# Kernel optimization log

Measured on AMD Instinct MI355X. Metric: run time of the kernel, lower is better.

Reference implementation:

```python
import jax, jax.numpy as jnp
import numpy as np
import math

B = 1024      # graphs
N = 64        # nodes per graph (padded, masked by node_mask)
BN = B * N    # total nodes
EPG = 192     # directed edges per graph
E = B * EPG


def setup_inputs() -> dict:
    key = jax.random.key(0)
    ks = jax.random.split(key, 40)

    def nrm(k, shp, s=0.02):
        return (jax.random.normal(k, shp) * s).astype(jnp.float32)

    mol_batch_x = jax.random.normal(ks[0], (BN, 19), dtype=jnp.float32)
    offs = jnp.arange(B, dtype=jnp.int32) * N
    src = jax.random.randint(ks[1], (B, EPG), 0, N, dtype=jnp.int32) + offs[:, None]
    dst = jax.random.randint(ks[2], (B, EPG), 0, N, dtype=jnp.int32) + offs[:, None]
    mol_batch_edge_index = jnp.stack([src.reshape(-1), dst.reshape(-1)], axis=0)
    mol_batch_batch = jnp.repeat(jnp.arange(B, dtype=jnp.int32), N)
    text_features = jax.random.normal(ks[3], (B, 300), dtype=jnp.float32)
    timesteps = jax.random.uniform(ks[4], (B,), minval=0.0, maxval=1000.0, dtype=jnp.float32)
    node_mask = (jax.random.uniform(ks[5], (B, N)) > 0.1).astype(jnp.float32)

    p = {
        'W_tr': nrm(ks[6], (19, 300)),   'b_tr': jnp.zeros((300,), jnp.float32),
        'W_c1': nrm(ks[7], (300, 600)),  'b_c1': jnp.zeros((600,), jnp.float32),
        'W_c2': nrm(ks[8], (600, 600)),  'b_c2': jnp.zeros((600,), jnp.float32),
        'W_c3': nrm(ks[9], (600, 600)),  'b_c3': jnp.zeros((600,), jnp.float32),
        'W_h1': nrm(ks[10], (600, 600)), 'b_h1': jnp.zeros((600,), jnp.float32),
        'W_h2': nrm(ks[11], (600, 600)), 'b_h2': jnp.zeros((600,), jnp.float32),
        'W_h3': nrm(ks[12], (600, 300)), 'b_h3': jnp.zeros((300,), jnp.float32),
        'ln_g': jnp.ones((300,), jnp.float32), 'ln_b': jnp.zeros((300,), jnp.float32),
        'W_t1': nrm(ks[13], (128, 512)), 'b_t1': jnp.zeros((512,), jnp.float32),
        'W_t2': nrm(ks[14], (512, 512)), 'b_t2': jnp.zeros((512,), jnp.float32),
        'W_e':  nrm(ks[15], (512, 3000)), 'b_e': jnp.zeros((3000,), jnp.float32),
    }
    return dict(mol_batch_x=mol_batch_x, mol_batch_edge_index=mol_batch_edge_index,
                mol_batch_batch=mol_batch_batch, text_features=text_features,
                timesteps=timesteps, node_mask=node_mask, **p)


def timestep_embedding(t, dim=128, max_period=10000.0):
    half = dim // 2
    freqs = jnp.exp(-math.log(max_period) * jnp.arange(half, dtype=jnp.float32) / half)
    args = t[:, None] * freqs[None]                 # [B, half]
    return jnp.concatenate([jnp.cos(args), jnp.sin(args)], axis=-1)  # [B, dim]


def gcn_conv(x, W, b, src, dst, num_nodes):
    # PyG GCNConv: D^{-1/2} (A + I) D^{-1/2} X W + b, edge weights 1
    h = x @ W                                             # [BN, F]
    deg = jnp.zeros((num_nodes,), h.dtype).at[dst].add(1.0) + 1.0  # in-degree + self-loop
    inv_sqrt = jax.lax.rsqrt(deg)
    coef = inv_sqrt[src] * inv_sqrt[dst]                  # [E]
    agg = jax.ops.segment_sum(h[src] * coef[:, None], dst, num_segments=num_nodes)
    return agg + h * (1.0 / deg)[:, None] + b             # self-loop norm = 1/deg


def global_mean_pool(x, batch, num_graphs):
    sums = jax.ops.segment_sum(x, batch, num_segments=num_graphs)
    cnts = jax.ops.segment_sum(jnp.ones((x.shape[0],), x.dtype), batch, num_segments=num_graphs)
    return sums / jnp.maximum(cnts, 1.0)[:, None]


def layer_norm(x, g, b, eps=1e-5):
    mu = jnp.mean(x, axis=-1, keepdims=True)
    var = jnp.mean(jnp.square(x - mu), axis=-1, keepdims=True)
    return (x - mu) * jax.lax.rsqrt(var + eps) * g + b


def reference(mol_batch_x, mol_batch_edge_index, mol_batch_batch, text_features,
              timesteps, node_mask, W_tr, b_tr, W_c1, b_c1, W_c2, b_c2, W_c3, b_c3,
              W_h1, b_h1, W_h2, b_h2, W_h3, b_h3, ln_g, ln_b,
              W_t1, b_t1, W_t2, b_t2, W_e, b_e):
    num_nodes = mol_batch_x.shape[0]
    num_graphs = node_mask.shape[0]
    src, dst = mol_batch_edge_index[0], mol_batch_edge_index[1]

    # FiLM conditioning from timestep embedding
    emb = jax.nn.relu(timestep_embedding(timesteps, 128) @ W_t1 + b_t1) @ W_t2 + b_t2  # [B,512]
    emb_out = jax.nn.relu(emb) @ W_e + b_e                                             # [B,3000]
    s1, t1 = emb_out[:, 0:600], emb_out[:, 600:1200]
    s2, t2 = emb_out[:, 1200:1800], emb_out[:, 1800:2400]
    s3, t3 = emb_out[:, 2400:2700], emb_out[:, 2700:3000]

    # node transform + mask
    x = mol_batch_x @ W_tr + b_tr                     # [BN, 300]
    x = x * node_mask.reshape(-1, 1)

    # GCN stack
    x = jax.nn.relu(gcn_conv(x, W_c1, b_c1, src, dst, num_nodes))
    x = jax.nn.relu(gcn_conv(x, W_c2, b_c2, src, dst, num_nodes))
    x = gcn_conv(x, W_c3, b_c3, src, dst, num_nodes)  # [BN, 600]

    g = global_mean_pool(x, mol_batch_batch, num_graphs)  # [B, 600]
    g = jax.nn.relu(g @ W_h1 + b_h1)
    g = g * (1.0 + s1) + t1
    g = jax.nn.relu(g @ W_h2 + b_h2)
    g = g * (1.0 + s2) + t2
    g = g @ W_h3 + b_h3                                # [B, 300]
    g = g * (1.0 + s3) + t3
    g = layer_norm(g, ln_g, ln_b)
    return (g, text_features)
```

## Files before the change

### kernel.cpp

```cpp
#include <hip/hip_runtime.h>
#include <hip/hip_bf16.h>
#include <cstdint>
#include <cstddef>

static constexpr int B   = 1024;
static constexpr int N   = 64;
static constexpr int BN  = B * N;
static constexpr int EPG = 192;
static constexpr int E   = B * EPG;
static constexpr int FP  = 608;
static constexpr int KP1 = 320;
static constexpr int PMS = 80;
static constexpr int NCONV = 2560;

typedef __hip_bfloat16 bf16;
typedef __bf16 bf16x8 __attribute__((ext_vector_type(8)));
typedef __bf16 bf16x4 __attribute__((ext_vector_type(4)));
typedef float  f32x4  __attribute__((ext_vector_type(4)));

__device__ __forceinline__ void storeC(float* p, float v) { *p = v; }
__device__ __forceinline__ void storeC(bf16* p, float v) { *p = __float2bfloat16(v); }

__device__ __forceinline__ void llds16(const void* g, void* l) {
    __builtin_amdgcn_global_load_lds(
        (const __attribute__((address_space(1))) unsigned int*)g,
        (__attribute__((address_space(3))) unsigned int*)l,
        16, 0, 0);
}

template<bool RELU, bool FILM, typename CT>
__device__ __forceinline__ void g64_tile(
    const bf16* __restrict__ A, int lda,
    const bf16* __restrict__ Bt, int ldb,
    const float* __restrict__ bias,
    CT* __restrict__ C, int ldc, int Ncap,
    const bf16* __restrict__ fS, const bf16* __restrict__ fT, int fstride,
    int K, int m0, int n0, __bf16* As, __bf16* Bs, int tid)
{
    const int lane = tid & 63;
    const int w    = tid >> 6;
    const int wn   = w * 32;
    const int l15  = lane & 15;
    const int lhi  = lane >> 4;

    f32x4 acc[4][2] = {};

    for (int k0 = 0; k0 < K; k0 += 32) {
        {
            int row = tid >> 2, kc = tid & 3;
            char* la = (char*)As + (size_t)(w * 64) * 16;
            llds16(A + (size_t)(m0 + row) * lda + k0 + kc * 8, la);
        }
        #pragma unroll
        for (int t = 0; t < 2; ++t) {
            int ci  = t * 256 + tid;
            int row = ci >> 2, kc = ci & 3;
// ... 2 lines not shown
        }
        asm volatile("s_waitcnt vmcnt(0)" ::: "memory");
        __syncthreads();

        bf16x8 af[4], bg[2];
        #pragma unroll
        for (int i = 0; i < 4; ++i)
            af[i] = *(bf16x8*)(As + (i * 16 + l15) * 32 + lhi * 8);
        #pragma unroll
        for (int j = 0; j < 2; ++j)
            bg[j] = *(bf16x8*)(Bs + (wn + j * 16 + l15) * 32 + lhi * 8);
        #pragma unroll
        for (int i = 0; i < 4; ++i)
            #pragma unroll
            for (int j = 0; j < 2; ++j)
                acc[i][j] = __builtin_amdgcn_mfma_f32_16x16x32_bf16(
                    af[i], bg[j], acc[i][j], 0, 0, 0);
        __syncthreads();
    }

    #pragma unroll
    for (int i = 0; i < 4; ++i) {
        #pragma unroll
        for (int j = 0; j < 2; ++j) {
            int col = n0 + wn + j * 16 + l15;
            if (col < Ncap) {
                float bv = bias ? bias[col] : 0.f;
                #pragma unroll
                for (int e = 0; e < 4; ++e) {
                    int row = m0 + i * 16 + lhi * 4 + e;
                    float v = acc[i][j][e] + bv;
                    if (RELU) v = fmaxf(v, 0.f);
                    if (FILM) {
                        float sv = __bfloat162float(fS[(size_t)row * fstride + col]);
                        float tv = __bfloat162float(fT[(size_t)row * fstride + col]);
                        v = v * (1.f + sv) + tv;
                    }
                    storeC(&C[(size_t)row * ldc + col], v);
                }
            }
        }
    }
}

__device__ __attribute__((noinline)) void guest_g64(
    const bf16* gA, int glda, const bf16* gBt, int gldb,
    const float* gbias, bf16* gC, int gldc, int gNcap, int gK, int gnt,
    int t, char* lds, int tid)
{
    int mt2 = t / gnt, nt2 = t % gnt;
    g64_tile<true, false, bf16>(gA, glda, gBt, gldb, gbias, gC, gldc, gNcap,
                                nullptr, nullptr, 0, gK, mt2 * 64, nt2 * 128,
                                (__bf16*)lds, (__bf16*)(lds + 4096), tid);
}

template<bool RELU, bool FILM, typename CT>
__global__ __launch_bounds__(256) void gemm64(
    const bf16* __restrict__ A, int lda,
    const bf16* __restrict__ Bt, int ldb,
    const float* __restrict__ bias,
    CT* __restrict__ C, int ldc, int Ncap,
    const bf16* __restrict__ fS, const bf16* __restrict__ fT, int fstride,
    int K)
{
    __shared__ __align__(16) __bf16 As[64 * 32];
    __shared__ __align__(16) __bf16 Bs[128 * 32];
    g64_tile<RELU, FILM, CT>(A, lda, Bt, ldb, bias, C, ldc, Ncap,
                             fS, fT, fstride, K,
                             blockIdx.x * 64, blockIdx.y * 128, As, Bs,
                             threadIdx.x);
}

__global__ __launch_bounds__(256) void k_two_gemms(
    const bf16* __restrict__ A2b, const bf16* __restrict__ Wet,
    const float* __restrict__ b_e, bf16* __restrict__ EO,
    const bf16* __restrict__ Yv, const bf16* __restrict__ Wb3,
    const float* __restrict__ b_c3, bf16* __restrict__ G0)
{
    __shared__ __align__(16) __bf16 As[64 * 32];
    __shared__ __align__(16) __bf16 Bs[128 * 32];
    int bid = blockIdx.x;
    if (bid < 384) {
        int mt = bid / 24, nt = bid % 24;
        g64_tile<false, false, bf16>(A2b, 512, Wet, 512, b_e, EO, 3000, 3000,
                                     nullptr, nullptr, 0, 512,
                                     mt * 64, nt * 128, As, Bs, threadIdx.x);
    } else {
        int t = bid - 384;
        int mt = t / 5, nt = t % 5;
        g64_tile<false, false, bf16>(Yv, FP, Wb3, FP, b_c3, G0, FP, 600,
                                     nullptr, nullptr, 0, FP,
                                     mt * 64, nt * 128, As, Bs, threadIdx.x);
    }
}

__global__ __launch_bounds__(256) void conv1_gemm(
    const bf16* __restrict__ A,
    const bf16* __restrict__ Bt,
    const float* __restrict__ bias,
    bf16* __restrict__ X1,
    const bf16* __restrict__ gA, int glda,
    const bf16* __restrict__ gBt, int gldb,
    const float* __restrict__ gbias,
    bf16* __restrict__ gC, int gldc, int gNcap, int gK, int gnt)
{
    __shared__ __align__(16) char regA[17408];
    const int tid = threadIdx.x;
    const int bid = blockIdx.x;

    if (bid >= NCONV) {
        guest_g64(gA, glda, gBt, gldb, gbias, gC, gldc, gNcap, gK, gnt,
                  bid - NCONV, regA, tid);
        return;
    }

    __bf16* As = (__bf16*)regA;
    __bf16* Bs = (__bf16*)(regA + 8192);

    const int lane = tid & 63;
    const int w    = tid >> 6;
    const int wm   = (w & 1) * 64;
    const int wn   = (w >> 1) * 64;
    const int l15  = lane & 15;
    const int lhi  = lane >> 4;

    const int lid = bid >> 3;
    const int mt  = (bid & 7) * 64 + lid / 5;
    const int nt  = lid % 5;
    const int m0  = mt * 128;
    const int n0  = nt * 128;

    f32x4 acc[4][4] = {};
    for (int k0 = 0; k0 < KP1; k0 += 32) {
        #pragma unroll
        for (int t = 0; t < 2; ++t) {
            int ci  = t * 256 + w * 64 + lane;
            int row = ci >> 2, kc = ci & 3;
            char* la = (char*)As + (size_t)(t * 256 + w * 64) * 16;
            char* lb = (char*)Bs + (size_t)(t * 256 + w * 64) * 16;
            llds16(A  + (size_t)(m0 + row) * KP1 + k0 + kc * 8, la);
            llds16(Bt + (size_t)(n0 + row) * KP1 + k0 + kc * 8, lb);
        }
        asm volatile("s_waitcnt vmcnt(0)" ::: "memory");
        __syncthreads();

        bf16x8 af[4], bg[4];
        #pragma unroll
        for (int i = 0; i < 4; ++i)
            af[i] = *(bf16x8*)(As + (wm + i * 16 + l15) * 32 + lhi * 8);
        #pragma unroll
        for (int j = 0; j < 4; ++j)
            bg[j] = *(bf16x8*)(Bs + (wn + j * 16 + l15) * 32 + lhi * 8);
        #pragma unroll
        for (int i = 0; i < 4; ++i)
            #pragma unroll
            for (int j = 0; j < 4; ++j)
                acc[i][j] = __builtin_amdgcn_mfma_f32_16x16x32_bf16(
                    af[i], bg[j], acc[i][j], 0, 0, 0);
        __syncthreads();
    }

    #pragma unroll
    for (int i = 0; i < 4; ++i)
        #pragma unroll
        for (int j = 0; j < 4; ++j) {
            int col = n0 + wn + j * 16 + l15;
            if (col < FP) {
                float bv = (col < 600) ? bias[col] : 0.f;
                #pragma unroll
                for (int e = 0; e < 4; ++e) {
                    int row = m0 + wm + i * 16 + lhi * 4 + e;
                    float v = fmaxf(acc[i][j][e] + bv, 0.f);
                    X1[(size_t)row * FP + col] = __float2bfloat16(v);
                }
            }
        }
}

__global__ __launch_bounds__(256) void conv_fused_q(
    const bf16* __restrict__ A, int lda, int K,
    const bf16* __restrict__ Bt, int ldb,
    const bf16* __restrict__ Pmg,
    const float* __restrict__ bias,
    const float* __restrict__ qv,
    bf16* __restrict__ Y,
    const bf16* __restrict__ gA, int glda,
    const bf16* __restrict__ gBt, int gldb,
    const float* __restrict__ gbias,
    bf16* __restrict__ gC, int gldc, int gNcap, int gK, int gnt)
{
    __shared__ __align__(16) char regA[17408];
    __shared__ __align__(16) __bf16 Pm[128 * PMS];
    __shared__ float s_q[128];

    const int tid = threadIdx.x;
    const int bid = blockIdx.x;

    if (bid >= NCONV) {
        guest_g64(gA, glda, gBt, gldb, gbias, gC, gldc, gNcap, gK, gnt,
                  bid - NCONV, regA, tid);
        return;
    }

    __bf16* As = (__bf16*)regA;
    __bf16* Bs = (__bf16*)(regA + 8192);
    __bf16* Ts = (__bf16*)regA;

    const int lane = tid & 63;
    const int w    = tid >> 6;
    const int wm   = (w & 1) * 64;
    const int wn   = (w >> 1) * 64;
    const int l15  = lane & 15;
    const int lhi  = lane >> 4;

    const int lid = bid >> 3;
    const int mt  = (bid & 7) * 64 + lid / 5;
    const int nt  = lid % 5;
    const int m0  = mt * 128;
    const int n0  = nt * 128;

    #pragma unroll
    for (int i = 0; i < 5; ++i) {
        int cbase = w * 320 + i * 64;
        llds16(Pmg + (size_t)mt * (128 * PMS) + (size_t)(cbase + lane) * 8,
               (char*)Pm + (size_t)cbase * 16);
    }
// ... 37 lines not shown
            #pragma unroll
            for (int i = 0; i < 4; ++i)
                #pragma unroll
                for (int j = 0; j < 4; ++j) {
                    int c_local = j * 16 + l15;
                    int rbase   = wm + i * 16 + lhi * 4;
                    bf16x4 pk;
                    #pragma unroll
                    for (int e = 0; e < 4; ++e) pk[e] = (__bf16)acc[i][j][e];
                    *(bf16x4*)(Ts + c_local * 136 + rbase) = pk;
                }
        }
        __syncthreads();

        f32x4 acc2[4][2] = {};
        #pragma unroll
        for (int k0 = 0; k0 < 64; k0 += 32) {
            bf16x8 pa[4], hb[2];
            #pragma unroll
            for (int i = 0; i < 4; ++i)
                pa[i] = *(bf16x8*)(Pm + (g * 64 + i * 16 + l15) * PMS + k0 + lhi * 8);
            #pragma unroll
            for (int j = 0; j < 2; ++j)
                hb[j] = *(bf16x8*)(Ts + (nb * 32 + j * 16 + l15) * 136
                                      + g * 64 + k0 + lhi * 8);
            #pragma unroll
            for (int i = 0; i < 4; ++i)
                #pragma unroll
                for (int j = 0; j < 2; ++j)
                    acc2[i][j] = __builtin_amdgcn_mfma_f32_16x16x32_bf16(
                        pa[i], hb[j], acc2[i][j], 0, 0, 0);
        }
        #pragma unroll
        for (int j = 0; j < 2; ++j) {
            int col = n0 + h * 64 + nb * 32 + j * 16 + l15;
            float bv = (col < 600) ? bias[col] : 0.f;
            float yp = 0.f;
            #pragma unroll
            for (int i = 0; i < 4; ++i)
                #pragma unroll
                for (int e = 0; e < 4; ++e) {
                    float v = fmaxf(acc2[i][j][e] + bv, 0.f);
                    yp += s_q[g * 64 + i * 16 + lhi * 4 + e] * v;
                }
            yp += __shfl_xor(yp, 16, 64);
            yp += __shfl_xor(yp, 32, 64);
            if (lhi == 0 && col < FP)
                Y[(size_t)(mt * 2 + g) * FP + col] = __float2bfloat16(yp);
        }
        __syncthreads();
    }
}

struct WtJob  { const float* src; bf16* dst; int Ksrc, Nsrc, Kp, Np, blk0; };
struct PrepArgs {
    WtJob j[9];
    int nwt, te0, pp0, xtr0;
    const int*   ei;
    const float* ts;
    const float* xin; const float* Wtr; const float* btr; const float* mask;
    bf16* TE; bf16* Pmg; float* qv; bf16* PX0;
};

__global__ __launch_bounds__(256) void k_prep(PrepArgs a)
{
    __shared__ __align__(16) char sm[35840];
    const int bx  = blockIdx.x;
    const int tid = threadIdx.x;

    if (bx < a.nwt) {
        int ji = 0;
        while (ji < 8 && bx >= a.j[ji + 1].blk0) ++ji;
        WtJob jb = a.j[ji];
        int t  = bx - jb.blk0;
        int kt = (jb.Kp + 63) >> 6;
        int ti = t % kt, tj = t / kt;
        int kg0 = ti * 64, ng0 = tj * 64;
        float (*T)[65] = (float(*)[65])sm;
        #pragma unroll 4
        for (int r = 0; r < 16; ++r) {
            int kl = (tid >> 6) + r * 4, nl = tid & 63;
            int kg = kg0 + kl, ng = ng0 + nl;
            T[kl][nl] = (kg < jb.Ksrc && ng < jb.Nsrc)
                        ? jb.src[(size_t)kg * jb.Nsrc + ng] : 0.f;
        }
        __syncthreads();
        #pragma unroll 4
        for (int r = 0; r < 16; ++r) {
            int nl = (tid >> 6) + r * 4, kl = tid & 63;
            int ng = ng0 + nl, kg = kg0 + kl;
            if (ng < jb.Np && kg < jb.Kp)
                jb.dst[(size_t)ng * jb.Kp + kg] = __float2bfloat16(T[kl][nl]);
        }
    } else if (bx < a.pp0) {
        int idx = (bx - a.te0) * 256 + tid;
        int b = idx >> 7, jj = idx & 127;
        float tt = a.ts[b];
        int h = jj & 63;
        float freq = expf(-9.210340371976184f * (float)h / 64.f);
        float ang = tt * freq;
        a.TE[idx] = __float2bfloat16((jj < 64) ? cosf(ang) : sinf(ang));
    } else if (bx < a.xtr0) {
        int pr = bx - a.pp0;
        float* Pf   = (float*)sm;
        int*   cnt  = (int*)(sm + 32768);
        float* sQ   = (float*)(sm + 33280);
        float* sI   = (float*)(sm + 33792);
        float* sIvd = (float*)(sm + 34304);

        for (int idx = tid; idx < 8192; idx += 256) Pf[idx] = 0.f;
        if (tid < 128) cnt[tid] = 0;
        __syncthreads();
        for (int e = tid; e < 2 * EPG; e += 256) {
            int g  = (e >= EPG);
            int eg = (2 * pr + g) * EPG + (e - g * EPG);
            int ld = (a.ei[E + eg] & 63) + g * 64;
            atomicAdd(&cnt[ld], 1);
        }
        __syncthreads();
        if (tid < 128) {
            float d = (float)cnt[tid] + 1.0f;
            float iv = 1.f / d;
            sIvd[tid] = iv;
            sI[tid]   = rsqrtf(d);
            sQ[tid]   = iv;
        }
        __syncthreads();
        for (int e = tid; e < 2 * EPG; e += 256) {
            int g   = (e >= EPG);
            int eg  = (2 * pr + g) * EPG + (e - g * EPG);
            int lsl = a.ei[eg] & 63;
            int ldl = a.ei[E + eg] & 63;
            float cf = sI[g * 64 + lsl] * sI[g * 64 + ldl];
            atomicAdd(&Pf[(g * 64 + ldl) * 64 + lsl], cf);
            atomicAdd(&sQ[g * 64 + lsl], cf);
        }
        __syncthreads();
        if (tid < 128) {
            Pf[tid * 64 + (tid & 63)] += sIvd[tid];
            a.qv[pr * 128 + tid] = sQ[tid] * (1.f / 64.f);
        }
        __syncthreads();
        for (int idx = tid; idx < 128 * PMS; idx += 256) {
            int r = idx / PMS, k = idx - r * PMS;
            float v = (k < 64) ? Pf[r * 64 + k] : 0.f;
            a.Pmg[(size_t)pr * (128 * PMS) + idx] = __float2bfloat16(v);
        }
    } else {
        int g = bx - a.xtr0;
        float* Pf  = (float*)sm;
        float* Ws  = (float*)sm;
        float* xm  = (float*)(sm + 23104);
        float* xa  = (float*)(sm + 28224);
        float* isqv= (float*)(sm + 33344);
        float* ivdv= (float*)(sm + 33600);
        int*   cnt = (int*)  (sm + 33856);
        float* sb  = (float*)(sm + 34112);

        for (int idx = tid; idx < 4096; idx += 256) Pf[idx] = 0.f;
        if (tid < 64) cnt[tid] = 0;
        __syncthreads();
        for (int e = tid; e < EPG; e += 256)
            atomicAdd(&cnt[a.ei[E + g * EPG + e] & 63], 1);
        __syncthreads();
        if (tid < 64) {
            float d = (float)cnt[tid] + 1.0f;
            ivdv[tid] = 1.f / d;
            isqv[tid] = rsqrtf(d);
        }
        __syncthreads();
        for (int e = tid; e < EPG; e += 256) {
            int ls = a.ei[g * EPG + e] & 63;
            int ld = a.ei[E + g * EPG + e] & 63;
            atomicAdd(&Pf[ld * 64 + ls], isqv[ls] * isqv[ld]);
        }
        for (int idx = tid; idx < 64 * 20; idx += 256) {
            int n = idx / 20, j = idx - n * 20;
            float mv = a.mask[g * 64 + n];
            xm[idx] = (j < 19) ? mv * a.xin[(size_t)(g * 64 + n) * 19 + j] : mv;
        }
        __syncthreads();
        if (tid < 64) Pf[tid * 64 + tid] += ivdv[tid];
        __syncthreads();
        for (int idx = tid; idx < 64 * 20; idx += 256) {
            int r = idx / 20, j = idx - r * 20;
            float s = 0.f;
            #pragma unroll 8
            for (int s2 = 0; s2 < 64; ++s2)
                s += Pf[r * 64 + s2] * xm[s2 * 20 + j];
            xa[idx] = s;
        }
        __syncthreads();
        for (int idx = tid; idx < 19 * 304; idx += 256) {
            int k = idx / 304, c = idx - k * 304;
            Ws[idx] = (c < 300) ? a.Wtr[k * 300 + c] : 0.f;
        }
        for (int c = tid; c < 304; c += 256)
            sb[c] = (c < 300) ? a.btr[c] : 0.f;
        __syncthreads();
        int n  = tid >> 2;
        int c0 = tid & 3;
        float ba = xa[n * 20 + 19];
        for (int c = c0; c < 304; c += 4) {
            float acc = ba * sb[c];
            #pragma unroll
            for (int k = 0; k < 19; ++k)
                acc += xa[n * 20 + k] * Ws[k * 304 + c];
            a.PX0[(size_t)(g * 64 + n) * KP1 + c] = __float2bfloat16(acc);
        }
        bf16x8 z = {};
        for (int idx = tid; idx < 64 * 2; idx += 256) {
            int nn = idx >> 1, jv = idx & 1;
            *(bf16x8*)((__bf16*)a.PX0 + (size_t)(g * 64 + nn) * KP1 + 304 + jv * 8) = z;
        }
    }
}

__global__ __launch_bounds__(256) void k_ln_copy(const float* __restrict__ G,
                                                 const float* __restrict__ lg,
                                                 const float* __restrict__ lb,
                                                 const float* __restrict__ text,
                                                 float* __restrict__ out)
{
    int r = blockIdx.x;
    int tid = threadIdx.x;
    __shared__ float red[4];
    __shared__ float smu, svar;

    float v0 = (tid < 300) ? G[r * 300 + tid] : 0.f;
    float v1 = (tid + 256 < 300) ? G[r * 300 + tid + 256] : 0.f;
    float s = v0 + v1;
    #pragma unroll
    for (int o = 32; o > 0; o >>= 1) s += __shfl_down(s, o, 64);
    if ((tid & 63) == 0) red[tid >> 6] = s;
    __syncthreads();
    if (tid == 0) smu = (red[0] + red[1] + red[2] + red[3]) * (1.f / 300.f);
    __syncthreads();
    float mu = smu;
    float d0 = (tid < 300) ? v0 - mu : 0.f;
    float d1 = (tid + 256 < 300) ? v1 - mu : 0.f;
    s = d0 * d0 + d1 * d1;
    #pragma unroll
    for (int o = 32; o > 0; o >>= 1) s += __shfl_down(s, o, 64);
    if ((tid & 63) == 0) red[tid >> 6] = s;
    __syncthreads();
    if (tid == 0) svar = (red[0] + red[1] + red[2] + red[3]) * (1.f / 300.f);
    __syncthreads();
    float rstd = rsqrtf(svar + 1e-5f);
    if (tid < 300)
        out[r * 300 + tid] = d0 * rstd * lg[tid] + lb[tid];
    if (tid + 256 < 300)
        out[r * 300 + tid + 256] = d1 * rstd * lg[tid + 256] + lb[tid + 256];
    float* o2 = out + (size_t)B * 300;
    for (int c = tid; c < 300; c += 256)
        o2[(size_t)r * 300 + c] = text[(size_t)r * 300 + c];
}

extern "C" void kernel_launch(void* const* d_in, const int* in_sizes, int n_in,
                              void* d_out, int out_size, void* d_ws, size_t ws_size,
                              hipStream_t stream)
{
    const float* x_in  = (const float*)d_in[0];
    const int*   ei    = (const int*)d_in[1];
    const float* text  = (const float*)d_in[3];
    const float* tst   = (const float*)d_in[4];
    const float* mask  = (const float*)d_in[5];
    const float* W_tr  = (const float*)d_in[6];
    const float* b_tr  = (const float*)d_in[7];
    const float* W_c1  = (const float*)d_in[8];
    const float* b_c1  = (const float*)d_in[9];
    const float* W_c2  = (const float*)d_in[10];
    const float* b_c2  = (const float*)d_in[11];
    const float* W_c3  = (const float*)d_in[12];
    const float* b_c3  = (const float*)d_in[13];
    const float* W_h1  = (const float*)d_in[14];
    const float* b_h1  = (const float*)d_in[15];
    const float* W_h2  = (const float*)d_in[16];
    const float* b_h2  = (const float*)d_in[17];
    const float* W_h3  = (const float*)d_in[18];
    const float* b_h3  = (const float*)d_in[19];
    const float* ln_g  = (const float*)d_in[20];
    const float* ln_b  = (const float*)d_in[21];
    const float* W_t1  = (const float*)d_in[22];
    const float* b_t1  = (const float*)d_in[23];
    const float* W_t2  = (const float*)d_in[24];
    const float* b_t2  = (const float*)d_in[25];
    const float* W_e   = (const float*)d_in[26];
    const float* b_e   = (const float*)d_in[27];

    char* w = (char*)d_ws;
    size_t off = 0;
    auto carve = [&](size_t bytes) {
        void* p = w + off;
        off += (bytes + 255) & ~(size_t)255;
        return p;
    };
    bf16*  PX0    = (bf16*) carve((size_t)BN * KP1 * 2);
    bf16*  X1     = (bf16*) carve((size_t)BN * FP * 2);
    bf16*  Wb1    = (bf16*) carve((size_t)640 * KP1 * 2);
    bf16*  Wb2    = (bf16*) carve((size_t)640 * FP * 2);
    bf16*  Wb3    = (bf16*) carve((size_t)640 * FP * 2);
    bf16*  Wt1t   = (bf16*) carve((size_t)512 * 128 * 2);
    bf16*  Wt2t   = (bf16*) carve((size_t)512 * 512 * 2);
    bf16*  Wet    = (bf16*) carve((size_t)3072 * 512 * 2);
    bf16*  Wh1t   = (bf16*) carve((size_t)640 * FP * 2);
    bf16*  Wh2t   = (bf16*) carve((size_t)640 * FP * 2);
    bf16*  Wh3t   = (bf16*) carve((size_t)384 * FP * 2);
    bf16*  TE     = (bf16*) carve((size_t)B * 128 * 2);
    bf16*  A1b    = (bf16*) carve((size_t)B * 512 * 2);
    bf16*  A2b    = (bf16*) carve((size_t)B * 512 * 2);
    bf16*  EO     = (bf16*) carve((size_t)B * 3000 * 2);
    bf16*  Yv     = (bf16*) carve((size_t)B * FP * 2);
    bf16*  G0     = (bf16*) carve((size_t)B * FP * 2);
    bf16*  G1     = (bf16*) carve((size_t)B * FP * 2);
    bf16*  G2     = (bf16*) carve((size_t)B * FP * 2);
    float* G3     = (float*)carve((size_t)B * 300 * 4);
    bf16*  Pmg    = (bf16*) carve((size_t)512 * 128 * PMS * 2);
    float* qv     = (float*)carve((size_t)BN * 4);
    (void)ws_size; (void)in_sizes; (void)n_in; (void)out_size;

    float* out = (float*)d_out;

    PrepArgs pa;
    struct JD { const float* s; bf16* d; int Ks, Ns, Kp, Np; };
    JD jd[9] = {
        { W_c1, Wb1,  300, 600,  KP1, 640 },
        { W_c2, Wb2,  600, 600,  FP,  640 },
        { W_c3, Wb3,  600, 600,  FP,  640 },
        { W_t1, Wt1t, 128, 512,  128, 512 },
        { W_t2, Wt2t, 512, 512,  512, 512 },
        { W_e,  Wet,  512, 3000, 512, 3072 },
        { W_h1, Wh1t, 600, 600,  FP,  640 },
        { W_h2, Wh2t, 600, 600,  FP,  640 },
        { W_h3, Wh3t, 600, 300,  FP,  384 },
    };
    int cum = 0;
    for (int i = 0; i < 9; ++i) {
        int kt = (jd[i].Kp + 63) >> 6, nt = (jd[i].Np + 63) >> 6;
        pa.j[i] = { jd[i].s, jd[i].d, jd[i].Ks, jd[i].Ns, jd[i].Kp, jd[i].Np, cum };
        cum += kt * nt;
    }
    pa.nwt  = cum;
    pa.te0  = cum;       cum += (B * 128) / 256;
    pa.pp0  = cum;       cum += B / 2;
    pa.xtr0 = cum;       cum += B;
    pa.ei = ei; pa.ts = tst;
    pa.xin = x_in; pa.Wtr = W_tr; pa.btr = b_tr; pa.mask = mask;
    pa.TE = TE; pa.Pmg = Pmg; pa.qv = qv; pa.PX0 = PX0;
    k_prep<<<cum, 256, 0, stream>>>(pa);

    conv1_gemm<<<NCONV + 64, 256, 0, stream>>>(
        PX0, Wb1, b_c1, X1,
        TE, 128, Wt1t, 128, b_t1, A1b, 512, 512, 128, 4);

    conv_fused_q<<<NCONV + 64, 256, 0, stream>>>(
        X1, FP, FP, Wb2, FP, Pmg, b_c2, qv, Yv,
        A1b, 512, Wt2t, 512, b_t2, A2b, 512, 512, 512, 4);

    k_two_gemms<<<464, 256, 0, stream>>>(A2b, Wet, b_e, EO, Yv, Wb3, b_c3, G0);

    gemm64<true, true, bf16><<<dim3(16, 5), 256, 0, stream>>>(
        G0, FP, Wh1t, FP, b_h1, G1, FP, 600, EO + 0, EO + 600, 3000, FP);
    gemm64<true, true, bf16><<<dim3(16, 5), 256, 0, stream>>>(
        G1, FP, Wh2t, FP, b_h2, G2, FP, 600, EO + 1200, EO + 1800, 3000, FP);
    gemm64<false, true, float><<<dim3(16, 3), 256, 0, stream>>>(
        G2, FP, Wh3t, FP, b_h3, G3, 300, 300, EO + 2400, EO + 2700, 3000, FP);

    k_ln_copy<<<B, 256, 0, stream>>>(G3, ln_g, ln_b, text, out);
}
```

Measured before the change: 367.0 us.

## Defer weight prep into conv1 guest blocks and fuse tail into cooperative kernel

```diff
diff --git a/kernel.cpp b/kernel.cpp
--- a/kernel.cpp
+++ b/kernel.cpp
@@ -1,7 +1,10 @@
 #include <hip/hip_runtime.h>
 #include <hip/hip_bf16.h>
+#include <hip/hip_cooperative_groups.h>
 #include <cstdint>
 #include <cstddef>
+
+namespace cg = cooperative_groups;
 
 static constexpr int B   = 1024;
 static constexpr int N   = 64;
@@ -112,63 +115,102 @@
                                 (__bf16*)lds, (__bf16*)(lds + 4096), tid);
 }
 
-template<bool RELU, bool FILM, typename CT>
-__global__ __launch_bounds__(256) void gemm64(
-    const bf16* __restrict__ A, int lda,
-    const bf16* __restrict__ Bt, int ldb,
-    const float* __restrict__ bias,
-    CT* __restrict__ C, int ldc, int Ncap,
-    const bf16* __restrict__ fS, const bf16* __restrict__ fT, int fstride,
-    int K)
-{
-    __shared__ __align__(16) __bf16 As[64 * 32];
-    __shared__ __align__(16) __bf16 Bs[128 * 32];
-    g64_tile<RELU, FILM, CT>(A, lda, Bt, ldb, bias, C, ldc, Ncap,
-                             fS, fT, fstride, K,
-                             blockIdx.x * 64, blockIdx.y * 128, As, Bs,
-                             threadIdx.x);
-}
-
-__global__ __launch_bounds__(256) void k_two_gemms(
-    const bf16* __restrict__ A2b, const bf16* __restrict__ Wet,
-    const float* __restrict__ b_e, bf16* __restrict__ EO,
-    const bf16* __restrict__ Yv, const bf16* __restrict__ Wb3,
-    const float* __restrict__ b_c3, bf16* __restrict__ G0)
-{
-    __shared__ __align__(16) __bf16 As[64 * 32];
-    __shared__ __align__(16) __bf16 Bs[128 * 32];
-    int bid = blockIdx.x;
-    if (bid < 384) {
-        int mt = bid / 24, nt = bid % 24;
-        g64_tile<false, false, bf16>(A2b, 512, Wet, 512, b_e, EO, 3000, 3000,
-                                     nullptr, nullptr, 0, 512,
-                                     mt * 64, nt * 128, As, Bs, threadIdx.x);
-    } else {
-        int t = bid - 384;
-        int mt = t / 5, nt = t % 5;
-        g64_tile<false, false, bf16>(Yv, FP, Wb3, FP, b_c3, G0, FP, 600,
-                                     nullptr, nullptr, 0, FP,
-                                     mt * 64, nt * 128, As, Bs, threadIdx.x);
-    }
-}
-
-__global__ __launch_bounds__(256) void conv1_gemm(
-    const bf16* __restrict__ A,
-    const bf16* __restrict__ Bt,
-    const float* __restrict__ bias,
-    bf16* __restrict__ X1,
-    const bf16* __restrict__ gA, int glda,
-    const bf16* __restrict__ gBt, int gldb,
-    const float* __restrict__ gbias,
-    bf16* __restrict__ gC, int gldc, int gNcap, int gK, int gnt)
+struct WtJob { const float* src; bf16* dst; int Ksrc, Nsrc, Kp, Np, blk0; };
+
+__device__ __attribute__((noinline)) void guest_wt(WtJob jb, int t, char* lds, int tid)
+{
+    int kt = (jb.Kp + 63) >> 6;
+    int ti = t % kt, tj = t / kt;
+    int kg0 = ti * 64, ng0 = tj * 64;
+    float (*T)[65] = (float(*)[65])lds;
+    #pragma unroll 4
+    for (int r = 0; r < 16; ++r) {
+        int kl = (tid >> 6) + r * 4, nl = tid & 63;
+        int kg = kg0 + kl, ng = ng0 + nl;
+        T[kl][nl] = (kg < jb.Ksrc && ng < jb.Nsrc)
+                    ? jb.src[(size_t)kg * jb.Nsrc + ng] : 0.f;
+    }
+    __syncthreads();
+    #pragma unroll 4
+    for (int r = 0; r < 16; ++r) {
+        int nl = (tid >> 6) + r * 4, kl = tid & 63;
+        int ng = ng0 + nl, kg = kg0 + kl;
+        if (ng < jb.Np && kg < jb.Kp)
+            jb.dst[(size_t)ng * jb.Kp + kg] = __float2bfloat16(T[kl][nl]);
+    }
+}
+
+__device__ __attribute__((noinline)) void guest_pp(
+    const int* ei, bf16* Pmg, float* qv, int g, char* lds, int tid)
+{
+    float* Pf   = (float*)lds;
+    int*   cnt  = (int*)  (lds + 16384);
+    float* sI   = (float*)(lds + 16640);
+    float* sIvd = (float*)(lds + 16896);
+    float* sQ   = (float*)(lds + 17152);
+
+    for (int i = tid; i < 4096; i += 256) Pf[i] = 0.f;
+    if (tid < 64) cnt[tid] = 0;
+    __syncthreads();
+    if (tid < EPG) atomicAdd(&cnt[ei[E + g * EPG + tid] & 63], 1);
+    __syncthreads();
+    if (tid < 64) {
+        float d = (float)cnt[tid] + 1.f;
+        float iv = 1.f / d;
+        sIvd[tid] = iv;
+        sI[tid]   = rsqrtf(d);
+        sQ[tid]   = iv;
+    }
+    __syncthreads();
+    if (tid < EPG) {
+        int ls = ei[g * EPG + tid] & 63;
+        int ld = ei[E + g * EPG + tid] & 63;
+        float cf = sI[ls] * sI[ld];
+        atomicAdd(&Pf[ld * 64 + ls], cf);
+        atomicAdd(&sQ[ls], cf);
+    }
+    __syncthreads();
+    if (tid < 64) {
+        Pf[tid * 64 + tid] += sIvd[tid];
+        qv[g * 64 + tid] = sQ[tid] * (1.f / 64.f);
+    }
+    __syncthreads();
+    int pr = g >> 1, half = g & 1;
+    for (int idx = tid; idx < 64 * PMS; idx += 256) {
+        int r = idx / PMS, k = idx - r * PMS;
+        float v = (k < 64) ? Pf[r * 64 + k] : 0.f;
+        Pmg[(size_t)pr * (128 * PMS) + (size_t)(half * 64 + r) * PMS + k]
+            = __float2bfloat16(v);
+    }
+}
+
+struct Conv1Args {
+    const bf16* A; const bf16* Bt; const float* bias; bf16* X1;
+    const bf16* TE; const bf16* Wt1t; const float* b_t1; bf16* A1b;
+    WtJob wj[7];
+    const int* ei; bf16* Pmg; float* qv;
+    int t1_end, wt_end;
+};
+
+__global__ __launch_bounds__(256) void conv1_gemm(Conv1Args a)
 {
     __shared__ __align__(16) char regA[17408];
     const int tid = threadIdx.x;
     const int bid = blockIdx.x;
 
     if (bid >= NCONV) {
-        guest_g64(gA, glda, gBt, gldb, gbias, gC, gldc, gNcap, gK, gnt,
-                  bid - NCONV, regA, tid);
+        int t = bid - NCONV;
+        if (t < a.t1_end) {
+            guest_g64(a.TE, 128, a.Wt1t, 128, a.b_t1, a.A1b, 512, 512, 128, 4,
+                      t, regA, tid);
+        } else if (t < a.wt_end) {
+            int tw = t - a.t1_end;
+            int ji = 0;
+            while (ji < 6 && tw >= a.wj[ji + 1].blk0) ++ji;
+            guest_wt(a.wj[ji], tw - a.wj[ji].blk0, regA, tid);
+        } else {
+            guest_pp(a.ei, a.Pmg, a.qv, t - a.wt_end, regA, tid);
+        }
         return;
     }
 
@@ -196,8 +238,8 @@
             int row = ci >> 2, kc = ci & 3;
             char* la = (char*)As + (size_t)(t * 256 + w * 64) * 16;
             char* lb = (char*)Bs + (size_t)(t * 256 + w * 64) * 16;
-            llds16(A  + (size_t)(m0 + row) * KP1 + k0 + kc * 8, la);
-            llds16(Bt + (size_t)(n0 + row) * KP1 + k0 + kc * 8, lb);
+            llds16(a.A  + (size_t)(m0 + row) * KP1 + k0 + kc * 8, la);
+            llds16(a.Bt + (size_t)(n0 + row) * KP1 + k0 + kc * 8, lb);
         }
         asm volatile("s_waitcnt vmcnt(0)" ::: "memory");
         __syncthreads();
@@ -224,12 +266,12 @@
         for (int j = 0; j < 4; ++j) {
             int col = n0 + wn + j * 16 + l15;
             if (col < FP) {
-                float bv = (col < 600) ? bias[col] : 0.f;
+                float bv = (col < 600) ? a.bias[col] : 0.f;
                 #pragma unroll
                 for (int e = 0; e < 4; ++e) {
                     int row = m0 + wm + i * 16 + lhi * 4 + e;
                     float v = fmaxf(acc[i][j][e] + bv, 0.f);
-                    X1[(size_t)row * FP + col] = __float2bfloat16(v);
+                    a.X1[(size_t)row * FP + col] = __float2bfloat16(v);
                 }
             }
         }
@@ -373,47 +415,25 @@
     }
 }
 
-struct WtJob  { const float* src; bf16* dst; int Ksrc, Nsrc, Kp, Np, blk0; };
-struct PrepArgs {
-    WtJob j[9];
-    int nwt, te0, pp0, xtr0;
+struct PrepAArgs {
+    WtJob j[2];
+    int nwt, te0;
     const int*   ei;
     const float* ts;
     const float* xin; const float* Wtr; const float* btr; const float* mask;
-    bf16* TE; bf16* Pmg; float* qv; bf16* PX0;
+    bf16* TE; bf16* PX0;
 };
 
-__global__ __launch_bounds__(256) void k_prep(PrepArgs a)
+__global__ __launch_bounds__(256) void prep_a(PrepAArgs a)
 {
     __shared__ __align__(16) char sm[35840];
     const int bx  = blockIdx.x;
     const int tid = threadIdx.x;
 
     if (bx < a.nwt) {
-        int ji = 0;
-        while (ji < 8 && bx >= a.j[ji + 1].blk0) ++ji;
-        WtJob jb = a.j[ji];
-        int t  = bx - jb.blk0;
-        int kt = (jb.Kp + 63) >> 6;
-        int ti = t % kt, tj = t / kt;
-        int kg0 = ti * 64, ng0 = tj * 64;
-        float (*T)[65] = (float(*)[65])sm;
-        #pragma unroll 4
-        for (int r = 0; r < 16; ++r) {
-            int kl = (tid >> 6) + r * 4, nl = tid & 63;
-            int kg = kg0 + kl, ng = ng0 + nl;
-            T[kl][nl] = (kg < jb.Ksrc && ng < jb.Nsrc)
-                        ? jb.src[(size_t)kg * jb.Nsrc + ng] : 0.f;
-        }
-        __syncthreads();
-        #pragma unroll 4
-        for (int r = 0; r < 16; ++r) {
-            int nl = (tid >> 6) + r * 4, kl = tid & 63;
-            int ng = ng0 + nl, kg = kg0 + kl;
-            if (ng < jb.Np && kg < jb.Kp)
-                jb.dst[(size_t)ng * jb.Kp + kg] = __float2bfloat16(T[kl][nl]);
-        }
-    } else if (bx < a.pp0) {
+        int ji = (bx >= a.j[1].blk0) ? 1 : 0;
+        guest_wt(a.j[ji], bx - a.j[ji].blk0, sm, tid);
+    } else if (bx < a.te0 + 512) {
         int idx = (bx - a.te0) * 256 + tid;
         int b = idx >> 7, jj = idx & 127;
         float tt = a.ts[b];
@@ -421,54 +441,8 @@
         float freq = expf(-9.210340371976184f * (float)h / 64.f);
         float ang = tt * freq;
         a.TE[idx] = __float2bfloat16((jj < 64) ? cosf(ang) : sinf(ang));
-    } else if (bx < a.xtr0) {
-        int pr = bx - a.pp0;
-        float* Pf   = (float*)sm;
-        int*   cnt  = (int*)(sm + 32768);
-        float* sQ   = (float*)(sm + 33280);
-        float* sI   = (float*)(sm + 33792);
-        float* sIvd = (float*)(sm + 34304);
-
-        for (int idx = tid; idx < 8192; idx += 256) Pf[idx] = 0.f;
-        if (tid < 128) cnt[tid] = 0;
-        __syncthreads();
-        for (int e = tid; e < 2 * EPG; e += 256) {
-            int g  = (e >= EPG);
-            int eg = (2 * pr + g) * EPG + (e - g * EPG);
-            int ld = (a.ei[E + eg] & 63) + g * 64;
-            atomicAdd(&cnt[ld], 1);
-        }
-        __syncthreads();
-        if (tid < 128) {
-            float d = (float)cnt[tid] + 1.0f;
-            float iv = 1.f / d;
-            sIvd[tid] = iv;
-            sI[tid]   = rsqrtf(d);
-            sQ[tid]   = iv;
-        }
-        __syncthreads();
-        for (int e = tid; e < 2 * EPG; e += 256) {
-            int g   = (e >= EPG);
-            int eg  = (2 * pr + g) * EPG + (e - g * EPG);
-            int lsl = a.ei[eg] & 63;
-            int ldl = a.ei[E + eg] & 63;
-            float cf = sI[g * 64 + lsl] * sI[g * 64 + ldl];
-            atomicAdd(&Pf[(g * 64 + ldl) * 64 + lsl], cf);
-            atomicAdd(&sQ[g * 64 + lsl], cf);
-        }
-        __syncthreads();
-        if (tid < 128) {
-            Pf[tid * 64 + (tid & 63)] += sIvd[tid];
-            a.qv[pr * 128 + tid] = sQ[tid] * (1.f / 64.f);
-        }
-        __syncthreads();
-        for (int idx = tid; idx < 128 * PMS; idx += 256) {
-            int r = idx / PMS, k = idx - r * PMS;
-            float v = (k < 64) ? Pf[r * 64 + k] : 0.f;
-            a.Pmg[(size_t)pr * (128 * PMS) + idx] = __float2bfloat16(v);
-        }
     } else {
-        int g = bx - a.xtr0;
+        int g = bx - (a.te0 + 512);
         float* Pf  = (float*)sm;
         float* Ws  = (float*)sm;
         float* xm  = (float*)(sm + 23104);
@@ -481,8 +455,7 @@
         for (int idx = tid; idx < 4096; idx += 256) Pf[idx] = 0.f;
         if (tid < 64) cnt[tid] = 0;
         __syncthreads();
-        for (int e = tid; e < EPG; e += 256)
-            atomicAdd(&cnt[a.ei[E + g * EPG + e] & 63], 1);
+        if (tid < EPG) atomicAdd(&cnt[a.ei[E + g * EPG + tid] & 63], 1);
         __syncthreads();
         if (tid < 64) {
             float d = (float)cnt[tid] + 1.0f;
@@ -490,9 +463,9 @@
             isqv[tid] = rsqrtf(d);
         }
         __syncthreads();
-        for (int e = tid; e < EPG; e += 256) {
-            int ls = a.ei[g * EPG + e] & 63;
-            int ld = a.ei[E + g * EPG + e] & 63;
+        if (tid < EPG) {
+            int ls = a.ei[g * EPG + tid] & 63;
+            int ld = a.ei[E + g * EPG + tid] & 63;
             atomicAdd(&Pf[ld * 64 + ls], isqv[ls] * isqv[ld]);
         }
         for (int idx = tid; idx < 64 * 20; idx += 256) {
@@ -537,44 +510,96 @@
     }
 }
 
-__global__ __launch_bounds__(256) void k_ln_copy(const float* __restrict__ G,
-                                                 const float* __restrict__ lg,
-                                                 const float* __restrict__ lb,
-                                                 const float* __restrict__ text,
-                                                 float* __restrict__ out)
-{
-    int r = blockIdx.x;
-    int tid = threadIdx.x;
+struct TailArgs {
+    const bf16* A2b; const bf16* Wet; const float* b_e; bf16* EO;
+    const bf16* Yv;  const bf16* Wb3; const float* b_c3; bf16* G0;
+    const bf16* Wh1t; const float* b_h1; bf16* G1;
+    const bf16* Wh2t; const float* b_h2; bf16* G2;
+    const bf16* Wh3t; const float* b_h3; float* G3;
+    const float* ln_g; const float* ln_b; const float* text; float* out;
+};
+
+__global__ __launch_bounds__(256) void k_tail(TailArgs a)
+{
+    __shared__ __align__(16) __bf16 As[64 * 32];
+    __shared__ __align__(16) __bf16 Bs[128 * 32];
     __shared__ float red[4];
     __shared__ float smu, svar;
 
-    float v0 = (tid < 300) ? G[r * 300 + tid] : 0.f;
-    float v1 = (tid + 256 < 300) ? G[r * 300 + tid + 256] : 0.f;
-    float s = v0 + v1;
-    #pragma unroll
-    for (int o = 32; o > 0; o >>= 1) s += __shfl_down(s, o, 64);
-    if ((tid & 63) == 0) red[tid >> 6] = s;
-    __syncthreads();
-    if (tid == 0) smu = (red[0] + red[1] + red[2] + red[3]) * (1.f / 300.f);
-    __syncthreads();
-    float mu = smu;
-    float d0 = (tid < 300) ? v0 - mu : 0.f;
-    float d1 = (tid + 256 < 300) ? v1 - mu : 0.f;
-    s = d0 * d0 + d1 * d1;
-    #pragma unroll
-    for (int o = 32; o > 0; o >>= 1) s += __shfl_down(s, o, 64);
-    if ((tid & 63) == 0) red[tid >> 6] = s;
-    __syncthreads();
-    if (tid == 0) svar = (red[0] + red[1] + red[2] + red[3]) * (1.f / 300.f);
-    __syncthreads();
-    float rstd = rsqrtf(svar + 1e-5f);
-    if (tid < 300)
-        out[r * 300 + tid] = d0 * rstd * lg[tid] + lb[tid];
-    if (tid + 256 < 300)
-        out[r * 300 + tid + 256] = d1 * rstd * lg[tid + 256] + lb[tid + 256];
-    float* o2 = out + (size_t)B * 300;
-    for (int c = tid; c < 300; c += 256)
-        o2[(size_t)r * 300 + c] = text[(size_t)r * 300 + c];
+    cg::grid_group grid = cg::this_grid();
+    const int bid = blockIdx.x;
+    const int tid = threadIdx.x;
+
+    for (int t = bid; t < 464; t += 384) {
+        if (t < 384) {
+            int mt = t / 24, nt = t % 24;
+            g64_tile<false, false, bf16>(a.A2b, 512, a.Wet, 512, a.b_e, a.EO,
+                                         3000, 3000, nullptr, nullptr, 0, 512,
+                                         mt * 64, nt * 128, As, Bs, tid);
+        } else {
+            int t2 = t - 384;
+            int mt = t2 / 5, nt = t2 % 5;
+            g64_tile<false, false, bf16>(a.Yv, FP, a.Wb3, FP, a.b_c3, a.G0,
+                                         FP, 600, nullptr, nullptr, 0, FP,
+                                         mt * 64, nt * 128, As, Bs, tid);
+        }
+    }
+    grid.sync();
+
+    if (bid < 80) {
+        int mt = bid / 5, nt = bid % 5;
+        g64_tile<true, true, bf16>(a.G0, FP, a.Wh1t, FP, a.b_h1, a.G1, FP, 600,
+                                   a.EO + 0, a.EO + 600, 3000, FP,
+                                   mt * 64, nt * 128, As, Bs, tid);
+    }
+    grid.sync();
+
+    if (bid < 80) {
+        int mt = bid / 5, nt = bid % 5;
+        g64_tile<true, true, bf16>(a.G1, FP, a.Wh2t, FP, a.b_h2, a.G2, FP, 600,
+                                   a.EO + 1200, a.EO + 1800, 3000, FP,
+                                   mt * 64, nt * 128, As, Bs, tid);
+    }
+    grid.sync();
+
+    if (bid < 48) {
+        int mt = bid / 3, nt = bid % 3;
+        g64_tile<false, true, float>(a.G2, FP, a.Wh3t, FP, a.b_h3, a.G3, 300, 300,
+                                     a.EO + 2400, a.EO + 2700, 3000, FP,
+                                     mt * 64, nt * 128, As, Bs, tid);
+    }
+    grid.sync();
+
+    for (int r = bid; r < B; r += 384) {
+        float v0 = (tid < 300) ? a.G3[r * 300 + tid] : 0.f;
+        float v1 = (tid + 256 < 300) ? a.G3[r * 300 + tid + 256] : 0.f;
+        float s = v0 + v1;
+        #pragma unroll
+        for (int o = 32; o > 0; o >>= 1) s += __shfl_down(s, o, 64);
+        if ((tid & 63) == 0) red[tid >> 6] = s;
+        __syncthreads();
+        if (tid == 0) smu = (red[0] + red[1] + red[2] + red[3]) * (1.f / 300.f);
+        __syncthreads();
+        float mu = smu;
+        float d0 = (tid < 300) ? v0 - mu : 0.f;
+        float d1 = (tid + 256 < 300) ? v1 - mu : 0.f;
+        s = d0 * d0 + d1 * d1;
+        #pragma unroll
+        for (int o = 32; o > 0; o >>= 1) s += __shfl_down(s, o, 64);
+        if ((tid & 63) == 0) red[tid >> 6] = s;
+        __syncthreads();
+        if (tid == 0) svar = (red[0] + red[1] + red[2] + red[3]) * (1.f / 300.f);
+        __syncthreads();
+        float rstd = rsqrtf(svar + 1e-5f);
+        if (tid < 300)
+            a.out[r * 300 + tid] = d0 * rstd * a.ln_g[tid] + a.ln_b[tid];
+        if (tid + 256 < 300)
+            a.out[r * 300 + tid + 256] = d1 * rstd * a.ln_g[tid + 256] + a.ln_b[tid + 256];
+        float* o2 = a.out + (size_t)B * 300;
+        for (int c = tid; c < 300; c += 256)
+            o2[(size_t)r * 300 + c] = a.text[(size_t)r * 300 + c];
+        __syncthreads();
+    }
 }
 
 extern "C" void kernel_launch(void* const* d_in, const int* in_sizes, int n_in,
@@ -642,50 +667,43 @@
 
     float* out = (float*)d_out;
 
-    PrepArgs pa;
-    struct JD { const float* s; bf16* d; int Ks, Ns, Kp, Np; };
-    JD jd[9] = {
-        { W_c1, Wb1,  300, 600,  KP1, 640 },
-        { W_c2, Wb2,  600, 600,  FP,  640 },
-        { W_c3, Wb3,  600, 600,  FP,  640 },
-        { W_t1, Wt1t, 128, 512,  128, 512 },
-        { W_t2, Wt2t, 512, 512,  512, 512 },
-        { W_e,  Wet,  512, 3000, 512, 3072 },
-        { W_h1, Wh1t, 600, 600,  FP,  640 },
-        { W_h2, Wh2t, 600, 600,  FP,  640 },
-        { W_h3, Wh3t, 600, 300,  FP,  384 },
-    };
-    int cum = 0;
-    for (int i = 0; i < 9; ++i) {
-        int kt = (jd[i].Kp + 63) >> 6, nt = (jd[i].Np + 63) >> 6;
-        pa.j[i] = { jd[i].s, jd[i].d, jd[i].Ks, jd[i].Ns, jd[i].Kp, jd[i].Np, cum };
-        cum += kt * nt;
-    }
-    pa.nwt  = cum;
-    pa.te0  = cum;       cum += (B * 128) / 256;
-    pa.pp0  = cum;       cum += B / 2;
-    pa.xtr0 = cum;       cum += B;
-    pa.ei = ei; pa.ts = tst;
-    pa.xin = x_in; pa.Wtr = W_tr; pa.btr = b_tr; pa.mask = mask;
-    pa.TE = TE; pa.Pmg = Pmg; pa.qv = qv; pa.PX0 = PX0;
-    k_prep<<<cum, 256, 0, stream>>>(pa);
-
-    conv1_gemm<<<NCONV + 64, 256, 0, stream>>>(
-        PX0, Wb1, b_c1, X1,
-        TE, 128, Wt1t, 128, b_t1, A1b, 512, 512, 128, 4);
+    PrepAArgs pp;
+    pp.j[0] = { W_c1, Wb1, 300, 600, KP1, 640, 0 };
+    pp.j[1] = { W_t1, Wt1t, 128, 512, 128, 512, 50 };
+    pp.nwt = 66;
+    pp.te0 = 66;
+    pp.ei = ei; pp.ts = tst;
+    pp.xin = x_in; pp.Wtr = W_tr; pp.btr = b_tr; pp.mask = mask;
+    pp.TE = TE; pp.PX0 = PX0;
+    prep_a<<<66 + 512 + B, 256, 0, stream>>>(pp);
+
+    Conv1Args c1;
+    c1.A = PX0; c1.Bt = Wb1; c1.bias = b_c1; c1.X1 = X1;
+    c1.TE = TE; c1.Wt1t = Wt1t; c1.b_t1 = b_t1; c1.A1b = A1b;
+    c1.wj[0] = { W_c2, Wb2,  600, 600,  FP,  640,  0   };
+    c1.wj[1] = { W_c3, Wb3,  600, 600,  FP,  640,  100 };
+    c1.wj[2] = { W_t2, Wt2t, 512, 512,  512, 512,  200 };
+    c1.wj[3] = { W_e,  Wet,  512, 3000, 512, 3072, 264 };
+    c1.wj[4] = { W_h1, Wh1t, 600, 600,  FP,  640,  648 };
+    c1.wj[5] = { W_h2, Wh2t, 600, 600,  FP,  640,  748 };
+    c1.wj[6] = { W_h3, Wh3t, 600, 300,  FP,  384,  848 };
+    c1.ei = ei; c1.Pmg = Pmg; c1.qv = qv;
+    c1.t1_end = 64;
+    c1.wt_end = 64 + 908;
+    conv1_gemm<<<NCONV + 64 + 908 + B, 256, 0, stream>>>(c1);
 
     conv_fused_q<<<NCONV + 64, 256, 0, stream>>>(
         X1, FP, FP, Wb2, FP, Pmg, b_c2, qv, Yv,
         A1b, 512, Wt2t, 512, b_t2, A2b, 512, 512, 512, 4);
 
-    k_two_gemms<<<464, 256, 0, stream>>>(A2b, Wet, b_e, EO, Yv, Wb3, b_c3, G0);
-
-    gemm64<true, true, bf16><<<dim3(16, 5), 256, 0, stream>>>(
-        G0, FP, Wh1t, FP, b_h1, G1, FP, 600, EO + 0, EO + 600, 3000, FP);
-    gemm64<true, true, bf16><<<dim3(16, 5), 256, 0, stream>>>(
-        G1, FP, Wh2t, FP, b_h2, G2, FP, 600, EO + 1200, EO + 1800, 3000, FP);
-    gemm64<false, true, float><<<dim3(16, 3), 256, 0, stream>>>(
-        G2, FP, Wh3t, FP, b_h3, G3, 300, 300, EO + 2400, EO + 2700, 3000, FP);
-
-    k_ln_copy<<<B, 256, 0, stream>>>(G3, ln_g, ln_b, text, out);
-}
+    TailArgs ta;
+    ta.A2b = A2b; ta.Wet = Wet; ta.b_e = b_e; ta.EO = EO;
+    ta.Yv = Yv; ta.Wb3 = Wb3; ta.b_c3 = b_c3; ta.G0 = G0;
+    ta.Wh1t = Wh1t; ta.b_h1 = b_h1; ta.G1 = G1;
+    ta.Wh2t = Wh2t; ta.b_h2 = b_h2; ta.G2 = G2;
+    ta.Wh3t = Wh3t; ta.b_h3 = b_h3; ta.G3 = G3;
+    ta.ln_g = ln_g; ta.ln_b = ln_b; ta.text = text; ta.out = out;
+    void* kargs[] = { (void*)&ta };
+    hipLaunchCooperativeKernel((void*)k_tail, dim3(384), dim3(256),
+                               kargs, 0, stream);
+}
```

New measurement: 599.3 us. 1.63x slower.

## Fuse head MLP GEMMs and layernorm into one row-block kernel

Applied to the files above, without the earlier changes.

```diff
diff --git a/kernel.cpp b/kernel.cpp
--- a/kernel.cpp
+++ b/kernel.cpp
@@ -110,23 +110,6 @@
     g64_tile<true, false, bf16>(gA, glda, gBt, gldb, gbias, gC, gldc, gNcap,
                                 nullptr, nullptr, 0, gK, mt2 * 64, nt2 * 128,
                                 (__bf16*)lds, (__bf16*)(lds + 4096), tid);
-}
-
-template<bool RELU, bool FILM, typename CT>
-__global__ __launch_bounds__(256) void gemm64(
-    const bf16* __restrict__ A, int lda,
-    const bf16* __restrict__ Bt, int ldb,
-    const float* __restrict__ bias,
-    CT* __restrict__ C, int ldc, int Ncap,
-    const bf16* __restrict__ fS, const bf16* __restrict__ fT, int fstride,
-    int K)
-{
-    __shared__ __align__(16) __bf16 As[64 * 32];
-    __shared__ __align__(16) __bf16 Bs[128 * 32];
-    g64_tile<RELU, FILM, CT>(A, lda, Bt, ldb, bias, C, ldc, Ncap,
-                             fS, fT, fstride, K,
-                             blockIdx.x * 64, blockIdx.y * 128, As, Bs,
-                             threadIdx.x);
 }
 
 __global__ __launch_bounds__(256) void k_two_gemms(
@@ -152,6 +135,99 @@
     }
 }
 
+struct HmlpArgs {
+    const bf16* G0; const bf16* Wh1t; const float* b_h1; bf16* G1;
+    const bf16* Wh2t; const float* b_h2; bf16* G2;
+    const bf16* Wh3t; const float* b_h3; float* G3;
+    const bf16* EO;
+    const float* ln_g; const float* ln_b; const float* text; float* out;
+};
+
+__global__ __launch_bounds__(1024) void k_hmlp(HmlpArgs a)
+{
+    __shared__ __align__(16) char lds[4][12288];
+    const int tid  = threadIdx.x;
+    const int grp  = tid >> 8;
+    const int ltid = tid & 255;
+    const int m0   = blockIdx.x * 64;
+    __bf16* As = (__bf16*)lds[grp];
+    __bf16* Bs = (__bf16*)(lds[grp] + 4096);
+
+    #pragma unroll
+    for (int rd = 0; rd < 2; ++rd) {
+        int t   = rd * 4 + grp;
+        int n0  = (t < 5) ? t * 128 : 512;
+        int cap = (t < 5) ? 600 : 0;
+        g64_tile<true, true, bf16>(a.G0, FP, a.Wh1t, FP, a.b_h1, a.G1, FP, cap,
+                                   a.EO + 0, a.EO + 600, 3000, FP,
+                                   m0, n0, As, Bs, ltid);
+    }
+    asm volatile("s_waitcnt vmcnt(0)" ::: "memory");
+    __syncthreads();
+
+    #pragma unroll
+    for (int rd = 0; rd < 2; ++rd) {
+        int t   = rd * 4 + grp;
+        int n0  = (t < 5) ? t * 128 : 512;
+        int cap = (t < 5) ? 600 : 0;
+        g64_tile<true, true, bf16>(a.G1, FP, a.Wh2t, FP, a.b_h2, a.G2, FP, cap,
+                                   a.EO + 1200, a.EO + 1800, 3000, FP,
+                                   m0, n0, As, Bs, ltid);
+    }
+    asm volatile("s_waitcnt vmcnt(0)" ::: "memory");
+    __syncthreads();
+
+    {
+        int t   = (grp < 3) ? grp : 2;
+        int cap = (grp < 3) ? 300 : 0;
+        g64_tile<false, true, float>(a.G2, FP, a.Wh3t, FP, a.b_h3, a.G3, 300, cap,
+                                     a.EO + 2400, a.EO + 2700, 3000, FP,
+                                     m0, t * 128, As, Bs, ltid);
+    }
+    asm volatile("s_waitcnt vmcnt(0)" ::: "memory");
+    __syncthreads();
+
+    const int wid  = tid >> 6;
+    const int lane = tid & 63;
+    #pragma unroll
+    for (int q = 0; q < 4; ++q) {
+        int r = m0 + wid * 4 + q;
+        float v[5];
+        float s = 0.f;
+        #pragma unroll
+        for (int k = 0; k < 5; ++k) {
+            int c = lane + 64 * k;
+            v[k] = (c < 300) ? a.G3[(size_t)r * 300 + c] : 0.f;
+            s += v[k];
+        }
+        #pragma unroll
+        for (int o = 32; o > 0; o >>= 1) s += __shfl_down(s, o, 64);
+        float mu = __shfl(s, 0, 64) * (1.f / 300.f);
+        float s2 = 0.f;
+        #pragma unroll
+        for (int k = 0; k < 5; ++k) {
+            int c = lane + 64 * k;
+            float d = (c < 300) ? v[k] - mu : 0.f;
+            v[k] = d;
+            s2 += d * d;
+        }
+        #pragma unroll
+        for (int o = 32; o > 0; o >>= 1) s2 += __shfl_down(s2, o, 64);
+        float rstd = rsqrtf(__shfl(s2, 0, 64) * (1.f / 300.f) + 1e-5f);
+        #pragma unroll
+        for (int k = 0; k < 5; ++k) {
+            int c = lane + 64 * k;
+            if (c < 300)
+                a.out[(size_t)r * 300 + c] = v[k] * rstd * a.ln_g[c] + a.ln_b[c];
+        }
+    }
+    float* o2 = a.out + (size_t)B * 300;
+    for (int idx = tid; idx < 64 * 300; idx += 1024) {
+        int rr = idx / 300, cc = idx - rr * 300;
+        o2[(size_t)(m0 + rr) * 300 + cc] = a.text[(size_t)(m0 + rr) * 300 + cc];
+    }
+}
+
 __global__ __launch_bounds__(256) void conv1_gemm(
     const bf16* __restrict__ A,
     const bf16* __restrict__ Bt,
@@ -481,8 +557,7 @@
         for (int idx = tid; idx < 4096; idx += 256) Pf[idx] = 0.f;
         if (tid < 64) cnt[tid] = 0;
         __syncthreads();
-        for (int e = tid; e < EPG; e += 256)
-            atomicAdd(&cnt[a.ei[E + g * EPG + e] & 63], 1);
+        if (tid < EPG) atomicAdd(&cnt[a.ei[E + g * EPG + tid] & 63], 1);
         __syncthreads();
         if (tid < 64) {
             float d = (float)cnt[tid] + 1.0f;
@@ -490,9 +565,9 @@
             isqv[tid] = rsqrtf(d);
         }
         __syncthreads();
-        for (int e = tid; e < EPG; e += 256) {
-            int ls = a.ei[g * EPG + e] & 63;
-            int ld = a.ei[E + g * EPG + e] & 63;
+        if (tid < EPG) {
+            int ls = a.ei[g * EPG + tid] & 63;
+            int ld = a.ei[E + g * EPG + tid] & 63;
             atomicAdd(&Pf[ld * 64 + ls], isqv[ls] * isqv[ld]);
         }
         for (int idx = tid; idx < 64 * 20; idx += 256) {
@@ -535,46 +610,6 @@
             *(bf16x8*)((__bf16*)a.PX0 + (size_t)(g * 64 + nn) * KP1 + 304 + jv * 8) = z;
         }
     }
-}
-
-__global__ __launch_bounds__(256) void k_ln_copy(const float* __restrict__ G,
-                                                 const float* __restrict__ lg,
-                                                 const float* __restrict__ lb,
-                                                 const float* __restrict__ text,
-                                                 float* __restrict__ out)
-{
-    int r = blockIdx.x;
-    int tid = threadIdx.x;
-    __shared__ float red[4];
-    __shared__ float smu, svar;
-
-    float v0 = (tid < 300) ? G[r * 300 + tid] : 0.f;
-    float v1 = (tid + 256 < 300) ? G[r * 300 + tid + 256] : 0.f;
-    float s = v0 + v1;
-    #pragma unroll
-    for (int o = 32; o > 0; o >>= 1) s += __shfl_down(s, o, 64);
-    if ((tid & 63) == 0) red[tid >> 6] = s;
-    __syncthreads();
-    if (tid == 0) smu = (red[0] + red[1] + red[2] + red[3]) * (1.f / 300.f);
-    __syncthreads();
-    float mu = smu;
-    float d0 = (tid < 300) ? v0 - mu : 0.f;
-    float d1 = (tid + 256 < 300) ? v1 - mu : 0.f;
-    s = d0 * d0 + d1 * d1;
-    #pragma unroll
-    for (int o = 32; o > 0; o >>= 1) s += __shfl_down(s, o, 64);
-    if ((tid & 63) == 0) red[tid >> 6] = s;
-    __syncthreads();
-    if (tid == 0) svar = (red[0] + red[1] + red[2] + red[3]) * (1.f / 300.f);
-    __syncthreads();
-    float rstd = rsqrtf(svar + 1e-5f);
-    if (tid < 300)
-        out[r * 300 + tid] = d0 * rstd * lg[tid] + lb[tid];
-    if (tid + 256 < 300)
-        out[r * 300 + tid + 256] = d1 * rstd * lg[tid + 256] + lb[tid + 256];
-    float* o2 = out + (size_t)B * 300;
-    for (int c = tid; c < 300; c += 256)
-        o2[(size_t)r * 300 + c] = text[(size_t)r * 300 + c];
 }
 
 extern "C" void kernel_launch(void* const* d_in, const int* in_sizes, int n_in,
@@ -680,12 +715,10 @@
 
     k_two_gemms<<<464, 256, 0, stream>>>(A2b, Wet, b_e, EO, Yv, Wb3, b_c3, G0);
 
-    gemm64<true, true, bf16><<<dim3(16, 5), 256, 0, stream>>>(
-        G0, FP, Wh1t, FP, b_h1, G1, FP, 600, EO + 0, EO + 600, 3000, FP);
-    gemm64<true, true, bf16><<<dim3(16, 5), 256, 0, stream>>>(
-        G1, FP, Wh2t, FP, b_h2, G2, FP, 600, EO + 1200, EO + 1800, 3000, FP);
-    gemm64<false, true, float><<<dim3(16, 3), 256, 0, stream>>>(
-        G2, FP, Wh3t, FP, b_h3, G3, 300, 300, EO + 2400, EO + 2700, 3000, FP);
-
-    k_ln_copy<<<B, 256, 0, stream>>>(G3, ln_g, ln_b, text, out);
-}
+    HmlpArgs hm;
+    hm.G0 = G0; hm.Wh1t = Wh1t; hm.b_h1 = b_h1; hm.G1 = G1;
+    hm.Wh2t = Wh2t; hm.b_h2 = b_h2; hm.G2 = G2;
+    hm.Wh3t = Wh3t; hm.b_h3 = b_h3; hm.G3 = G3;
+    hm.EO = EO; hm.ln_g = ln_g; hm.ln_b = ln_b; hm.text = text; hm.out = out;
+    k_hmlp<<<16, 1024, 0, stream>>>(hm);
+}
```

Result: slower. 525.1 us (+43.1%).
